# Optimization experiments

Measured on AMD Instinct MI355X. Metric: run time of the kernel, lower is better.

## Reference

```python
import jax, jax.numpy as jnp
import numpy as np

N_NODES = 50000
N_EDGES = 400000
N_TRAIN = 50000
IN_DIM = 128
HIDDEN = 512


def gcn_conv(x, W, b, src, dst, num_nodes):
    """PyG-style GCNConv: linear -> add self-loops -> sym-normalized scatter-add -> bias."""
    h = x @ W  # [N, out]
    loop = jnp.arange(num_nodes, dtype=src.dtype)
    src2 = jnp.concatenate([src, loop])  # self-loops appended
    dst2 = jnp.concatenate([dst, loop])
    ones = jnp.ones(src2.shape[0], dtype=h.dtype)
    deg = jax.ops.segment_sum(ones, dst2, num_segments=num_nodes)  # in-degree incl. self-loop
    dis = jnp.where(deg > 0, jax.lax.rsqrt(deg), 0.0)
    norm = dis[src2] * dis[dst2]  # [E+N]
    msgs = h[src2] * norm[:, None]  # [E+N, out] gather
    out = jax.ops.segment_sum(msgs, dst2, num_segments=num_nodes)  # scatter-add
    return out + b


def setup_inputs() -> dict:
    key = jax.random.key(0)
    ks = jax.random.split(key, 12)
    x = jax.random.normal(ks[0], (N_NODES, IN_DIM), dtype=jnp.float32)
    edge_index = jax.random.randint(ks[1], (2, N_EDGES), 0, N_NODES, dtype=jnp.int32)
    train_edge_id = jax.random.randint(ks[2], (N_TRAIN,), 0, N_EDGES, dtype=jnp.int32)
    def glorot(k, fi, fo):
        s = (6.0 / (fi + fo)) ** 0.5
        return jax.random.uniform(k, (fi, fo), jnp.float32, -s, s)
    return {
        "x": x,
        "edge_index": edge_index,
        "train_edge_id": train_edge_id,
        "W1": glorot(ks[3], IN_DIM, HIDDEN), "b1": jnp.zeros((HIDDEN,), jnp.float32),
        "W2": glorot(ks[4], HIDDEN, HIDDEN), "b2": jnp.zeros((HIDDEN,), jnp.float32),
        "W3": glorot(ks[5], HIDDEN, HIDDEN), "b3": jnp.zeros((HIDDEN,), jnp.float32),
        "fc2_W": glorot(ks[6], HIDDEN, 1), "fc2_b": jnp.zeros((1,), jnp.float32),
    }


def reference(x, edge_index, train_edge_id, W1, b1, W2, b2, W3, b3, fc2_W, fc2_b):
    src, dst = edge_index[0], edge_index[1]
    n = x.shape[0]
    h = jnp.tanh(gcn_conv(x, W1, b1, src, dst, n))
    h = jnp.tanh(gcn_conv(h, W2, b2, src, dst, n))
    h = jnp.tanh(gcn_conv(h, W3, b3, src, dst, n))
    # dropout is identity in eval mode
    node_id = edge_index[:, train_edge_id]  # [2, T]
    e = h[node_id[0]] * h[node_id[1]]  # [T, HIDDEN] edge gather + mul
    return e @ fc2_W + fc2_b  # [T, 1]
```

## Files before the change

### kernel.cpp

```cpp
#include <hip/hip_runtime.h>
#include <math.h>

#define N_NODES 50000
#define N_EDGES 400000
#define N_TRAIN 50000
#define IN_DIM  128
#define HIDDEN  512
#define M_PAD   50048
#define SCAN_B  196

typedef _Float16 f16;
typedef __attribute__((ext_vector_type(8))) _Float16 f16x8;
typedef __attribute__((ext_vector_type(4))) _Float16 f16x4;
typedef __attribute__((ext_vector_type(4))) float f32x4;


__global__ void count_dst_kernel(const int* __restrict__ dst, int* __restrict__ cnt) {
    int i = blockIdx.x * blockDim.x + threadIdx.x;
    if (i < N_EDGES) atomicAdd(&cnt[dst[i]], 1);
}

__global__ void dis_kernel(const int* __restrict__ cnt, float* __restrict__ dis) {
    int v = blockIdx.x * blockDim.x + threadIdx.x;
    if (v < N_NODES) dis[v] = rsqrtf(1.0f + (float)cnt[v]);
}

__global__ void scan1_kernel(const int* __restrict__ cnt, int* __restrict__ bsum) {
    __shared__ int red[256];
    int t = threadIdx.x, i = blockIdx.x * 256 + t;
    red[t] = (i < N_NODES) ? cnt[i] : 0;
    __syncthreads();
    for (int o = 128; o > 0; o >>= 1) {
        if (t < o) red[t] += red[t + o];
        __syncthreads();
    }
    if (t == 0) bsum[blockIdx.x] = red[0];
}

__global__ void scan2_kernel(const int* __restrict__ bsum, int* __restrict__ boff) {
    __shared__ int part[256];
    int t = threadIdx.x;
    int v = (t < SCAN_B) ? bsum[t] : 0;
    part[t] = v;
    __syncthreads();
    for (int o = 1; o < 256; o <<= 1) {
        int u = (t >= o) ? part[t - o] : 0;
        __syncthreads();
        part[t] += u;
        __syncthreads();
    }
    if (t < SCAN_B) boff[t] = part[t] - v;
}

__global__ void scan3_kernel(const int* __restrict__ cnt, const int* __restrict__ boff,
                             int* __restrict__ off) {
    __shared__ int part[256];
    int t = threadIdx.x, i = blockIdx.x * 256 + t;
    int v = (i < N_NODES) ? cnt[i] : 0;
    part[t] = v;
    __syncthreads();
    for (int o = 1; o < 256; o <<= 1) {
        int u = (t >= o) ? part[t - o] : 0;
        __syncthreads();
        part[t] += u;
        __syncthreads();
    }
    int excl = part[t] - v;
    int base = boff[blockIdx.x];
    if (i < N_NODES) off[i] = base + excl;
    if (i == N_NODES - 1) off[N_NODES] = base + excl + v;
}

__global__ void fill_csr_kernel(const int* __restrict__ src, const int* __restrict__ dst,
                                const int* __restrict__ off, int* __restrict__ cursor,
                                const float* __restrict__ dis,
                                int* __restrict__ csr_src, float* __restrict__ csr_w) {
    int i = blockIdx.x * blockDim.x + threadIdx.x;
    if (i < N_EDGES) {
        int d = dst[i], s = src[i];
        int p = atomicAdd(&cursor[d], 1);
        int idx = off[d] + p;
        csr_src[idx] = s;
        csr_w[idx] = dis[s];
    }
}

__global__ void convw_kernel(const float* __restrict__ W, f16* __restrict__ Bt, int K) {
    int idx = blockIdx.x * blockDim.x + threadIdx.x;
    if (idx >= K * HIDDEN) return;
    int k = idx / HIDDEN, n = idx % HIDDEN;
    Bt[(size_t)n * K + k] = (f16)W[(size_t)k * HIDDEN + n];
}

__global__ void agg1_kernel(const float* __restrict__ x, const float* __restrict__ dis,
                            const int* __restrict__ off, const int* __restrict__ csr_src,
                            const float* __restrict__ csr_w, f16* __restrict__ A) {
    const int TPN = 32;
    int node = blockIdx.x * 8 + threadIdx.x / TPN;
    if (node >= N_NODES) return;
    int t = threadIdx.x % TPN;
    float dv = dis[node];
    float w0 = dv * dv;
    float4 a = ((const float4*)(x + (size_t)node * IN_DIM))[t];
    float4 acc = make_float4(a.x * w0, a.y * w0, a.z * w0, a.w * w0);
    float4 acc1 = make_float4(0.f, 0.f, 0.f, 0.f);
    int s0 = off[node], s1 = off[node + 1];
    int k = s0;
    for (; k + 2 <= s1; k += 2) {
        int sa = csr_src[k], sb = csr_src[k + 1];
        float wa = csr_w[k] * dv, wb = csr_w[k + 1] * dv;
        float4 ba = ((const float4*)(x + (size_t)sa * IN_DIM))[t];
        float4 bb = ((const float4*)(x + (size_t)sb * IN_DIM))[t];
        acc.x = fmaf(wa, ba.x, acc.x);   acc.y = fmaf(wa, ba.y, acc.y);
        acc.z = fmaf(wa, ba.z, acc.z);   acc.w = fmaf(wa, ba.w, acc.w);
        acc1.x = fmaf(wb, bb.x, acc1.x); acc1.y = fmaf(wb, bb.y, acc1.y);
        acc1.z = fmaf(wb, bb.z, acc1.z); acc1.w = fmaf(wb, bb.w, acc1.w);
    }
    if (k < s1) {
        int sa = csr_src[k];
        float wa = csr_w[k] * dv;
        float4 ba = ((const float4*)(x + (size_t)sa * IN_DIM))[t];
        acc.x = fmaf(wa, ba.x, acc.x); acc.y = fmaf(wa, ba.y, acc.y);
        acc.z = fmaf(wa, ba.z, acc.z); acc.w = fmaf(wa, ba.w, acc.w);
    }
    f16x4 o;
    o.x = (f16)(acc.x + acc1.x); o.y = (f16)(acc.y + acc1.y);
    o.z = (f16)(acc.z + acc1.z); o.w = (f16)(acc.w + acc1.w);
    *(f16x4*)&A[(size_t)node * IN_DIM + t * 4] = o;
}

__global__ void agg_f16_kernel(const f16* __restrict__ h, const float* __restrict__ dis,
                               const int* __restrict__ off, const int* __restrict__ csr_src,
                               const float* __restrict__ csr_w, f16* __restrict__ A) {
    const int TPN = 64;
    int node = blockIdx.x * 4 + threadIdx.x / TPN;
    if (node >= N_NODES) return;
    int t = threadIdx.x % TPN;
    float dv = dis[node];
    float w0 = dv * dv;
    f16x8 a = *(const f16x8*)&h[(size_t)node * HIDDEN + t * 8];
    float acc0[8], acc1[8];
    #pragma unroll
    for (int j = 0; j < 8; j++) { acc0[j] = w0 * (float)a[j]; acc1[j] = 0.f; }
    int s0 = off[node], s1 = off[node + 1];
    int k = s0;
    for (; k + 8 <= s1; k += 8) {
        f16x8 b[8];
        float w[8];
        #pragma unroll
        for (int u = 0; u < 8; u++) {
            int su = csr_src[k + u];
            w[u] = csr_w[k + u] * dv;
            b[u] = *(const f16x8*)&h[(size_t)su * HIDDEN + t * 8];
        }
        #pragma unroll
        for (int j = 0; j < 8; j++) {
            acc0[j] = fmaf(w[0], (float)b[0][j], acc0[j]);
            acc1[j] = fmaf(w[1], (float)b[1][j], acc1[j]);
            acc0[j] = fmaf(w[2], (float)b[2][j], acc0[j]);
            acc1[j] = fmaf(w[3], (float)b[3][j], acc1[j]);
            acc0[j] = fmaf(w[4], (float)b[4][j], acc0[j]);
            acc1[j] = fmaf(w[5], (float)b[5][j], acc1[j]);
            acc0[j] = fmaf(w[6], (float)b[6][j], acc0[j]);
            acc1[j] = fmaf(w[7], (float)b[7][j], acc1[j]);
        }
    }
    if (k + 4 <= s1) {
        f16x8 b[4];
        float w[4];
        #pragma unroll
        for (int u = 0; u < 4; u++) {
            int su = csr_src[k + u];
            w[u] = csr_w[k + u] * dv;
            b[u] = *(const f16x8*)&h[(size_t)su * HIDDEN + t * 8];
        }
        #pragma unroll
        for (int j = 0; j < 8; j++) {
            acc0[j] = fmaf(w[0], (float)b[0][j], acc0[j]);
            acc1[j] = fmaf(w[1], (float)b[1][j], acc1[j]);
            acc0[j] = fmaf(w[2], (float)b[2][j], acc0[j]);
            acc1[j] = fmaf(w[3], (float)b[3][j], acc1[j]);
        }
        k += 4;
    }
    if (k + 2 <= s1) {
        int sa = csr_src[k], sb = csr_src[k + 1];
        float wa = csr_w[k] * dv, wb = csr_w[k + 1] * dv;
        f16x8 ba = *(const f16x8*)&h[(size_t)sa * HIDDEN + t * 8];
        f16x8 bb = *(const f16x8*)&h[(size_t)sb * HIDDEN + t * 8];
        #pragma unroll
        for (int j = 0; j < 8; j++) {
            acc0[j] = fmaf(wa, (float)ba[j], acc0[j]);
            acc1[j] = fmaf(wb, (float)bb[j], acc1[j]);
        }
        k += 2;
    }
    if (k < s1) {
        int sa = csr_src[k];
        float wa = csr_w[k] * dv;
        f16x8 ba = *(const f16x8*)&h[(size_t)sa * HIDDEN + t * 8];
        #pragma unroll
        for (int j = 0; j < 8; j++) acc0[j] = fmaf(wa, (float)ba[j], acc0[j]);
    }
    f16x8 o;
    #pragma unroll
    for (int j = 0; j < 8; j++) o[j] = (f16)(acc0[j] + acc1[j]);
    *(f16x8*)&A[(size_t)node * HIDDEN + t * 8] = o;
}

__global__ __launch_bounds__(256, 4) void gemm_mfma_kernel(
    const f16* __restrict__ A, const f16* __restrict__ Bt, const float* __restrict__ bias,
    f16* __restrict__ C, int M, int Kb) {
    __shared__ f16 smem[17408];
    f16* As = smem;
    f16* Bs = smem + 8192;
    int tid = threadIdx.x;
    int lane = tid & 63, wv = tid >> 6;
    int wr = wv >> 1, wc = wv & 1;

    int nwg = gridDim.x;
    int q = nwg >> 3, r = nwg & 7;
    int xcd = blockIdx.x & 7, pos = blockIdx.x >> 3;
    int wgid = (xcd < r ? xcd * (q + 1) : r * (q + 1) + (xcd - r) * q) + pos;
    int j0 = (wgid & 3) * 128;
    int i0 = (wgid >> 2) * 128;

    int l15 = lane & 15, l4 = lane >> 4;

    f32x4 acc[4][4];
    #pragma unroll
    for (int m = 0; m < 4; m++)
        #pragma unroll
        for (int n = 0; n < 4; n++)
            acc[m][n] = (f32x4){0.f, 0.f, 0.f, 0.f};

    const int nt = Kb / 64;
    for (int t = 0; t < nt; t++) {
        int k0 = t * 64;
        if (t) __syncthreads();
        #pragma unroll
        for (int i = 0; i < 4; i++) {
            int s = i * 256 + tid;
            int row = s >> 3, c8 = s & 7;
            int c8s = c8 ^ (row & 7);
            const f16* gp = A + (size_t)(i0 + row) * Kb + k0 + c8s * 8;
            f16* lp = &As[(i * 256 + wv * 64) * 8];
            __builtin_amdgcn_global_load_lds(
                (const __attribute__((address_space(1))) void*)gp,
                (__attribute__((address_space(3))) void*)lp, 16, 0, 0);
        }
        #pragma unroll
        for (int i = 0; i < 4; i++) {
            int s = i * 256 + tid;
            int row = s >> 3, c8 = s & 7;
            int c8s = c8 ^ (row & 7);
            const f16* gp = Bt + (size_t)(j0 + row) * Kb + k0 + c8s * 8;
            f16* lp = &Bs[(i * 256 + wv * 64) * 8];
            __builtin_amdgcn_global_load_lds(
                (const __attribute__((address_space(1))) void*)gp,
                (__attribute__((address_space(3))) void*)lp, 16, 0, 0);
        }
        __syncthreads();

        f16x8 af[4][2], bfr[4][2];
        #pragma unroll
        for (int m = 0; m < 4; m++) {
            int row = wr * 64 + m * 16 + l15;
            #pragma unroll
            for (int kk = 0; kk < 2; kk++) {
                int slot = (kk * 4 + l4) ^ (row & 7);
                af[m][kk] = *(const f16x8*)&As[row * 64 + slot * 8];
            }
        }
        #pragma unroll
        for (int n = 0; n < 4; n++) {
            int brow = wc * 64 + n * 16 + l15;
            #pragma unroll
            for (int kk = 0; kk < 2; kk++) {
                int slot = (kk * 4 + l4) ^ (brow & 7);
                bfr[n][kk] = *(const f16x8*)&Bs[brow * 64 + slot * 8];
            }
        }
        #pragma unroll
        for (int m = 0; m < 4; m++)
            #pragma unroll
            for (int n = 0; n < 4; n++)
                #pragma unroll
                for (int kk = 0; kk < 2; kk++)
                    acc[m][n] = __builtin_amdgcn_mfma_f32_16x16x32_f16(
                        af[m][kk], bfr[n][kk], acc[m][n], 0, 0, 0);
    }

    __syncthreads();
    #pragma unroll
    for (int m = 0; m < 4; m++) {
        #pragma unroll
        for (int n = 0; n < 4; n++) {
            int lcol = wc * 64 + n * 16 + l15;
            float bc = bias[j0 + lcol];
            #pragma unroll
            for (int rr = 0; rr < 4; rr++) {
                int lrow = wr * 64 + m * 16 + l4 * 4 + rr;
                smem[lrow * 136 + lcol] = (f16)tanhf(acc[m][n][rr] + bc);
            }
        }
    }
    __syncthreads();
    #pragma unroll
    for (int j = 0; j < 8; j++) {
        int qq = j * 256 + tid;
        int row = qq >> 4, c8 = qq & 15;
        int grow = i0 + row;
        if (grow < M)
            *(f16x8*)&C[(size_t)grow * HIDDEN + j0 + c8 * 8] =
                *(const f16x8*)&smem[row * 136 + c8 * 8];
    }
}

__global__ void edge_score_kernel(const f16* __restrict__ h,
                                  const int* __restrict__ src, const int* __restrict__ dst,
                                  const int* __restrict__ te, const float* __restrict__ wgt,
                                  const float* __restrict__ fc2b, float* __restrict__ out) {
    int wid = threadIdx.x / 64;
    int lane = threadIdx.x % 64;
    int e = blockIdx.x * 4 + wid;
    if (e >= N_TRAIN) return;
    int id = te[e];
    int a = src[id], b = dst[id];
    f16x8 ha = *(const f16x8*)&h[(size_t)a * HIDDEN + lane * 8];
    f16x8 hb = *(const f16x8*)&h[(size_t)b * HIDDEN + lane * 8];
    float4 w0 = *(const float4*)&wgt[lane * 8];
    float4 w1 = *(const float4*)&wgt[lane * 8 + 4];
    float acc = 0.f;
    acc += (float)ha[0] * (float)hb[0] * w0.x;
    acc += (float)ha[1] * (float)hb[1] * w0.y;
    acc += (float)ha[2] * (float)hb[2] * w0.z;
    acc += (float)ha[3] * (float)hb[3] * w0.w;
    acc += (float)ha[4] * (float)hb[4] * w1.x;
    acc += (float)ha[5] * (float)hb[5] * w1.y;
    acc += (float)ha[6] * (float)hb[6] * w1.z;
    acc += (float)ha[7] * (float)hb[7] * w1.w;
    #pragma unroll
    for (int o = 32; o > 0; o >>= 1) acc += __shfl_down(acc, o);
    if (lane == 0) out[e] = acc + fc2b[0];
}


extern "C" void kernel_launch(void* const* d_in, const int* in_sizes, int n_in,
                              void* d_out, int out_size, void* d_ws, size_t ws_size,
                              hipStream_t stream) {
    const float* x    = (const float*)d_in[0];
    const int*   eidx = (const int*)d_in[1];
    const int*   te   = (const int*)d_in[2];
    const float* W1   = (const float*)d_in[3];
    const float* b1   = (const float*)d_in[4];
    const float* W2   = (const float*)d_in[5];
    const float* b2   = (const float*)d_in[6];
    const float* W3   = (const float*)d_in[7];
    const float* b3   = (const float*)d_in[8];
    const float* fc2W = (const float*)d_in[9];
    const float* fc2b = (const float*)d_in[10];
    const int* srcp = eidx;
    const int* dstp = eidx + N_EDGES;

    char* ws = (char*)d_ws;
    size_t used = 0;
    auto alloc = [&](size_t bytes) {
        void* p = ws + used;
        used += (bytes + 255) / 256 * 256;
        return p;
    };
    int*   cnt     = (int*)alloc((size_t)N_NODES * 4);
    int*   off     = (int*)alloc((size_t)(N_NODES + 1) * 4);
    int*   cursor  = (int*)alloc((size_t)N_NODES * 4);
    int*   bsum    = (int*)alloc((size_t)SCAN_B * 4);
    int*   boff    = (int*)alloc((size_t)SCAN_B * 4);
    int*   csr_src = (int*)alloc((size_t)N_EDGES * 4);
    float* csr_w   = (float*)alloc((size_t)N_EDGES * 4);
    float* dis     = (float*)alloc((size_t)N_NODES * 4);
    f16* Bt1 = (f16*)alloc((size_t)HIDDEN * IN_DIM * 2);
    f16* Bt2 = (f16*)alloc((size_t)HIDDEN * HIDDEN * 2);
    f16* Bt3 = (f16*)alloc((size_t)HIDDEN * HIDDEN * 2);
    f16* GA  = (f16*)alloc((size_t)M_PAD * HIDDEN * 2);
    f16* F   = (f16*)alloc((size_t)M_PAD * HIDDEN * 2);

    if (used > ws_size) return;

    hipMemsetAsync(cnt, 0, (size_t)N_NODES * 4, stream);
    hipMemsetAsync(cursor, 0, (size_t)N_NODES * 4, stream);

    count_dst_kernel<<<(N_EDGES + 255) / 256, 256, 0, stream>>>(dstp, cnt);
    dis_kernel<<<(N_NODES + 255) / 256, 256, 0, stream>>>(cnt, dis);
    scan1_kernel<<<SCAN_B, 256, 0, stream>>>(cnt, bsum);
    scan2_kernel<<<1, 256, 0, stream>>>(bsum, boff);
    scan3_kernel<<<SCAN_B, 256, 0, stream>>>(cnt, boff, off);
    fill_csr_kernel<<<(N_EDGES + 255) / 256, 256, 0, stream>>>(srcp, dstp, off, cursor, dis,
                                                               csr_src, csr_w);

    convw_kernel<<<(IN_DIM * HIDDEN + 255) / 256, 256, 0, stream>>>(W1, Bt1, IN_DIM);
    convw_kernel<<<(HIDDEN * HIDDEN + 255) / 256, 256, 0, stream>>>(W2, Bt2, HIDDEN);
    convw_kernel<<<(HIDDEN * HIDDEN + 255) / 256, 256, 0, stream>>>(W3, Bt3, HIDDEN);

    int gemm_blocks = (HIDDEN / 128) * (M_PAD / 128);

    agg1_kernel<<<(N_NODES + 7) / 8, 256, 0, stream>>>(x, dis, off, csr_src, csr_w, GA);
    gemm_mfma_kernel<<<gemm_blocks, 256, 0, stream>>>(GA, Bt1, b1, F, N_NODES, IN_DIM);
    agg_f16_kernel<<<(N_NODES + 3) / 4, 256, 0, stream>>>(F, dis, off, csr_src, csr_w, GA);
    gemm_mfma_kernel<<<gemm_blocks, 256, 0, stream>>>(GA, Bt2, b2, F, N_NODES, HIDDEN);
    agg_f16_kernel<<<(N_NODES + 3) / 4, 256, 0, stream>>>(F, dis, off, csr_src, csr_w, GA);
    gemm_mfma_kernel<<<gemm_blocks, 256, 0, stream>>>(GA, Bt3, b3, F, N_NODES, HIDDEN);
    edge_score_kernel<<<(N_TRAIN + 3) / 4, 256, 0, stream>>>(F, srcp, dstp, te, fc2W, fc2b,
                                                             (float*)d_out);
}
```

Baseline: 357.8 us.

## Fuse preprocessing kernels, cast x to fp16, and use nontemporal stores

Merges the dis computation into the first scan pass and folds the block-offset scan into the final scan kernel. The three weight-conversion launches become one. x is cast to fp16 up front so the first aggregation reuses the templated fp16 gather kernel and moves half the bytes per neighbour. Stores from the aggregation and GEMM epilogue are made nontemporal. This cuts launch count and gather traffic, but adds an extra pass over x, and nontemporal stores may hurt when the next kernel reads the output soon after.

After: 359.3 us. Within noise of the previous version (+0.4%).

```diff
diff --git a/kernel.cpp b/kernel.cpp
--- a/kernel.cpp
+++ b/kernel.cpp
@@ -11,7 +11,6 @@
 
 typedef _Float16 f16;
 typedef __attribute__((ext_vector_type(8))) _Float16 f16x8;
-typedef __attribute__((ext_vector_type(4))) _Float16 f16x4;
 typedef __attribute__((ext_vector_type(4))) float f32x4;
 
 
@@ -20,15 +19,13 @@
     if (i < N_EDGES) atomicAdd(&cnt[dst[i]], 1);
 }
 
-__global__ void dis_kernel(const int* __restrict__ cnt, float* __restrict__ dis) {
-    int v = blockIdx.x * blockDim.x + threadIdx.x;
-    if (v < N_NODES) dis[v] = rsqrtf(1.0f + (float)cnt[v]);
-}
-
-__global__ void scan1_kernel(const int* __restrict__ cnt, int* __restrict__ bsum) {
+__global__ void scan1_dis_kernel(const int* __restrict__ cnt, int* __restrict__ bsum,
+                                 float* __restrict__ dis) {
     __shared__ int red[256];
     int t = threadIdx.x, i = blockIdx.x * 256 + t;
-    red[t] = (i < N_NODES) ? cnt[i] : 0;
+    int v = (i < N_NODES) ? cnt[i] : 0;
+    if (i < N_NODES) dis[i] = rsqrtf(1.0f + (float)v);
+    red[t] = v;
     __syncthreads();
     for (int o = 128; o > 0; o >>= 1) {
         if (t < o) red[t] += red[t + o];
@@ -37,10 +34,23 @@
     if (t == 0) bsum[blockIdx.x] = red[0];
 }
 
-__global__ void scan2_kernel(const int* __restrict__ bsum, int* __restrict__ boff) {
+__global__ void scan3_kernel(const int* __restrict__ cnt, const int* __restrict__ bsum,
+                             int* __restrict__ off) {
+    __shared__ int bpart[256];
     __shared__ int part[256];
     int t = threadIdx.x;
-    int v = (t < SCAN_B) ? bsum[t] : 0;
+    int bv = (t < SCAN_B) ? bsum[t] : 0;
+    bpart[t] = bv;
+    __syncthreads();
+    for (int o = 1; o < 256; o <<= 1) {
+        int u = (t >= o) ? bpart[t - o] : 0;
+        __syncthreads();
+        bpart[t] += u;
+        __syncthreads();
+    }
+    int base = (blockIdx.x > 0) ? bpart[blockIdx.x - 1] : 0;
+    int i = blockIdx.x * 256 + t;
+    int v = (i < N_NODES) ? cnt[i] : 0;
     part[t] = v;
     __syncthreads();
     for (int o = 1; o < 256; o <<= 1) {
@@ -49,24 +59,7 @@
         part[t] += u;
         __syncthreads();
     }
-    if (t < SCAN_B) boff[t] = part[t] - v;
-}
-
-__global__ void scan3_kernel(const int* __restrict__ cnt, const int* __restrict__ boff,
-                             int* __restrict__ off) {
-    __shared__ int part[256];
-    int t = threadIdx.x, i = blockIdx.x * 256 + t;
-    int v = (i < N_NODES) ? cnt[i] : 0;
-    part[t] = v;
-    __syncthreads();
-    for (int o = 1; o < 256; o <<= 1) {
-        int u = (t >= o) ? part[t - o] : 0;
-        __syncthreads();
-        part[t] += u;
-        __syncthreads();
-    }
     int excl = part[t] - v;
-    int base = boff[blockIdx.x];
     if (i < N_NODES) off[i] = base + excl;
     if (i == N_NODES - 1) off[N_NODES] = base + excl + v;
 }
@@ -85,60 +78,50 @@
     }
 }
 
-__global__ void convw_kernel(const float* __restrict__ W, f16* __restrict__ Bt, int K) {
+__global__ void convw_all_kernel(const float* __restrict__ W1, const float* __restrict__ W2,
+                                 const float* __restrict__ W3, f16* __restrict__ Bt1,
+                                 f16* __restrict__ Bt2, f16* __restrict__ Bt3) {
+    const int S1 = IN_DIM * HIDDEN;
+    const int S2 = S1 + HIDDEN * HIDDEN;
+    const int S3 = S2 + HIDDEN * HIDDEN;
     int idx = blockIdx.x * blockDim.x + threadIdx.x;
-    if (idx >= K * HIDDEN) return;
-    int k = idx / HIDDEN, n = idx % HIDDEN;
-    Bt[(size_t)n * K + k] = (f16)W[(size_t)k * HIDDEN + n];
-}
-
-__global__ void agg1_kernel(const float* __restrict__ x, const float* __restrict__ dis,
-                            const int* __restrict__ off, const int* __restrict__ csr_src,
-                            const float* __restrict__ csr_w, f16* __restrict__ A) {
-    const int TPN = 32;
-    int node = blockIdx.x * 8 + threadIdx.x / TPN;
+    if (idx >= S3) return;
+    if (idx < S1) {
+        int k = idx / HIDDEN, n = idx % HIDDEN;
+        Bt1[(size_t)n * IN_DIM + k] = (f16)W1[idx];
+    } else if (idx < S2) {
+        int j = idx - S1;
+        int k = j / HIDDEN, n = j % HIDDEN;
+        Bt2[(size_t)n * HIDDEN + k] = (f16)W2[j];
+    } else {
+        int j = idx - S2;
+        int k = j / HIDDEN, n = j % HIDDEN;
+        Bt3[(size_t)n * HIDDEN + k] = (f16)W3[j];
+    }
+}
+
+__global__ void xcast_kernel(const float* __restrict__ x, f16* __restrict__ XF) {
+    int i = blockIdx.x * blockDim.x + threadIdx.x;
+    if (i >= N_NODES * IN_DIM / 8) return;
+    const float4* p = (const float4*)x + (size_t)i * 2;
+    float4 a = p[0], b = p[1];
+    f16x8 o = {(f16)a.x, (f16)a.y, (f16)a.z, (f16)a.w,
+               (f16)b.x, (f16)b.y, (f16)b.z, (f16)b.w};
+    __builtin_nontemporal_store(o, (f16x8*)XF + i);
+}
+
+template <int D>
+__global__ void agg_kernel(const f16* __restrict__ h, const float* __restrict__ dis,
+                           const int* __restrict__ off, const int* __restrict__ csr_src,
+                           const float* __restrict__ csr_w, f16* __restrict__ A) {
+    const int TPN = D / 8;
+    const int NPB = 256 / TPN;
+    int node = blockIdx.x * NPB + threadIdx.x / TPN;
     if (node >= N_NODES) return;
     int t = threadIdx.x % TPN;
     float dv = dis[node];
     float w0 = dv * dv;
-    float4 a = ((const float4*)(x + (size_t)node * IN_DIM))[t];
-    float4 acc = make_float4(a.x * w0, a.y * w0, a.z * w0, a.w * w0);
-    float4 acc1 = make_float4(0.f, 0.f, 0.f, 0.f);
-    int s0 = off[node], s1 = off[node + 1];
-    int k = s0;
-    for (; k + 2 <= s1; k += 2) {
-        int sa = csr_src[k], sb = csr_src[k + 1];
-        float wa = csr_w[k] * dv, wb = csr_w[k + 1] * dv;
-        float4 ba = ((const float4*)(x + (size_t)sa * IN_DIM))[t];
-        float4 bb = ((const float4*)(x + (size_t)sb * IN_DIM))[t];
-        acc.x = fmaf(wa, ba.x, acc.x);   acc.y = fmaf(wa, ba.y, acc.y);
-        acc.z = fmaf(wa, ba.z, acc.z);   acc.w = fmaf(wa, ba.w, acc.w);
-        acc1.x = fmaf(wb, bb.x, acc1.x); acc1.y = fmaf(wb, bb.y, acc1.y);
-        acc1.z = fmaf(wb, bb.z, acc1.z); acc1.w = fmaf(wb, bb.w, acc1.w);
-    }
-    if (k < s1) {
-        int sa = csr_src[k];
-        float wa = csr_w[k] * dv;
-        float4 ba = ((const float4*)(x + (size_t)sa * IN_DIM))[t];
-        acc.x = fmaf(wa, ba.x, acc.x); acc.y = fmaf(wa, ba.y, acc.y);
-        acc.z = fmaf(wa, ba.z, acc.z); acc.w = fmaf(wa, ba.w, acc.w);
-    }
-    f16x4 o;
-    o.x = (f16)(acc.x + acc1.x); o.y = (f16)(acc.y + acc1.y);
-    o.z = (f16)(acc.z + acc1.z); o.w = (f16)(acc.w + acc1.w);
-    *(f16x4*)&A[(size_t)node * IN_DIM + t * 4] = o;
-}
-
-__global__ void agg_f16_kernel(const f16* __restrict__ h, const float* __restrict__ dis,
-                               const int* __restrict__ off, const int* __restrict__ csr_src,
-                               const float* __restrict__ csr_w, f16* __restrict__ A) {
-    const int TPN = 64;
-    int node = blockIdx.x * 4 + threadIdx.x / TPN;
-    if (node >= N_NODES) return;
-    int t = threadIdx.x % TPN;
-    float dv = dis[node];
-    float w0 = dv * dv;
-    f16x8 a = *(const f16x8*)&h[(size_t)node * HIDDEN + t * 8];
+    f16x8 a = *(const f16x8*)&h[(size_t)node * D + t * 8];
     float acc0[8], acc1[8];
     #pragma unroll
     for (int j = 0; j < 8; j++) { acc0[j] = w0 * (float)a[j]; acc1[j] = 0.f; }
@@ -151,7 +134,7 @@
         for (int u = 0; u < 8; u++) {
             int su = csr_src[k + u];
             w[u] = csr_w[k + u] * dv;
-            b[u] = *(const f16x8*)&h[(size_t)su * HIDDEN + t * 8];
+            b[u] = *(const f16x8*)&h[(size_t)su * D + t * 8];
         }
         #pragma unroll
         for (int j = 0; j < 8; j++) {
@@ -172,7 +155,7 @@
         for (int u = 0; u < 4; u++) {
             int su = csr_src[k + u];
             w[u] = csr_w[k + u] * dv;
-            b[u] = *(const f16x8*)&h[(size_t)su * HIDDEN + t * 8];
+            b[u] = *(const f16x8*)&h[(size_t)su * D + t * 8];
         }
         #pragma unroll
         for (int j = 0; j < 8; j++) {
@@ -186,8 +169,8 @@
     if (k + 2 <= s1) {
         int sa = csr_src[k], sb = csr_src[k + 1];
         float wa = csr_w[k] * dv, wb = csr_w[k + 1] * dv;
-        f16x8 ba = *(const f16x8*)&h[(size_t)sa * HIDDEN + t * 8];
-        f16x8 bb = *(const f16x8*)&h[(size_t)sb * HIDDEN + t * 8];
+        f16x8 ba = *(const f16x8*)&h[(size_t)sa * D + t * 8];
+        f16x8 bb = *(const f16x8*)&h[(size_t)sb * D + t * 8];
         #pragma unroll
         for (int j = 0; j < 8; j++) {
             acc0[j] = fmaf(wa, (float)ba[j], acc0[j]);
@@ -198,14 +181,14 @@
     if (k < s1) {
         int sa = csr_src[k];
         float wa = csr_w[k] * dv;
-        f16x8 ba = *(const f16x8*)&h[(size_t)sa * HIDDEN + t * 8];
+        f16x8 ba = *(const f16x8*)&h[(size_t)sa * D + t * 8];
         #pragma unroll
         for (int j = 0; j < 8; j++) acc0[j] = fmaf(wa, (float)ba[j], acc0[j]);
     }
     f16x8 o;
     #pragma unroll
     for (int j = 0; j < 8; j++) o[j] = (f16)(acc0[j] + acc1[j]);
-    *(f16x8*)&A[(size_t)node * HIDDEN + t * 8] = o;
+    __builtin_nontemporal_store(o, (f16x8*)&A[(size_t)node * D + t * 8]);
 }
 
 __global__ __launch_bounds__(256, 4) void gemm_mfma_kernel(
@@ -311,9 +294,10 @@
         int qq = j * 256 + tid;
         int row = qq >> 4, c8 = qq & 15;
         int grow = i0 + row;
-        if (grow < M)
-            *(f16x8*)&C[(size_t)grow * HIDDEN + j0 + c8 * 8] =
-                *(const f16x8*)&smem[row * 136 + c8 * 8];
+        if (grow < M) {
+            f16x8 v = *(const f16x8*)&smem[row * 136 + c8 * 8];
+            __builtin_nontemporal_store(v, (f16x8*)&C[(size_t)grow * HIDDEN + j0 + c8 * 8]);
+        }
     }
 }
 
@@ -374,13 +358,13 @@
     int*   off     = (int*)alloc((size_t)(N_NODES + 1) * 4);
     int*   cursor  = (int*)alloc((size_t)N_NODES * 4);
     int*   bsum    = (int*)alloc((size_t)SCAN_B * 4);
-    int*   boff    = (int*)alloc((size_t)SCAN_B * 4);
     int*   csr_src = (int*)alloc((size_t)N_EDGES * 4);
     float* csr_w   = (float*)alloc((size_t)N_EDGES * 4);
     float* dis     = (float*)alloc((size_t)N_NODES * 4);
     f16* Bt1 = (f16*)alloc((size_t)HIDDEN * IN_DIM * 2);
     f16* Bt2 = (f16*)alloc((size_t)HIDDEN * HIDDEN * 2);
     f16* Bt3 = (f16*)alloc((size_t)HIDDEN * HIDDEN * 2);
+    f16* XF  = (f16*)alloc((size_t)N_NODES * IN_DIM * 2);
     f16* GA  = (f16*)alloc((size_t)M_PAD * HIDDEN * 2);
     f16* F   = (f16*)alloc((size_t)M_PAD * HIDDEN * 2);
 
@@ -390,24 +374,23 @@
     hipMemsetAsync(cursor, 0, (size_t)N_NODES * 4, stream);
 
     count_dst_kernel<<<(N_EDGES + 255) / 256, 256, 0, stream>>>(dstp, cnt);
-    dis_kernel<<<(N_NODES + 255) / 256, 256, 0, stream>>>(cnt, dis);
-    scan1_kernel<<<SCAN_B, 256, 0, stream>>>(cnt, bsum);
-    scan2_kernel<<<1, 256, 0, stream>>>(bsum, boff);
-    scan3_kernel<<<SCAN_B, 256, 0, stream>>>(cnt, boff, off);
+    scan1_dis_kernel<<<SCAN_B, 256, 0, stream>>>(cnt, bsum, dis);
+    scan3_kernel<<<SCAN_B, 256, 0, stream>>>(cnt, bsum, off);
     fill_csr_kernel<<<(N_EDGES + 255) / 256, 256, 0, stream>>>(srcp, dstp, off, cursor, dis,
                                                                csr_src, csr_w);
-
-    convw_kernel<<<(IN_DIM * HIDDEN + 255) / 256, 256, 0, stream>>>(W1, Bt1, IN_DIM);
-    convw_kernel<<<(HIDDEN * HIDDEN + 255) / 256, 256, 0, stream>>>(W2, Bt2, HIDDEN);
-    convw_kernel<<<(HIDDEN * HIDDEN + 255) / 256, 256, 0, stream>>>(W3, Bt3, HIDDEN);
+    convw_all_kernel<<<(589824 + 255) / 256, 256, 0, stream>>>(W1, W2, W3, Bt1, Bt2, Bt3);
+    xcast_kernel<<<(N_NODES * IN_DIM / 8 + 255) / 256, 256, 0, stream>>>(x, XF);
 
     int gemm_blocks = (HIDDEN / 128) * (M_PAD / 128);
 
-    agg1_kernel<<<(N_NODES + 7) / 8, 256, 0, stream>>>(x, dis, off, csr_src, csr_w, GA);
+    agg_kernel<IN_DIM><<<(N_NODES + 15) / 16, 256, 0, stream>>>(XF, dis, off, csr_src,
+                                                                csr_w, GA);
     gemm_mfma_kernel<<<gemm_blocks, 256, 0, stream>>>(GA, Bt1, b1, F, N_NODES, IN_DIM);
-    agg_f16_kernel<<<(N_NODES + 3) / 4, 256, 0, stream>>>(F, dis, off, csr_src, csr_w, GA);
+    agg_kernel<HIDDEN><<<(N_NODES + 3) / 4, 256, 0, stream>>>(F, dis, off, csr_src,
+                                                              csr_w, GA);
     gemm_mfma_kernel<<<gemm_blocks, 256, 0, stream>>>(GA, Bt2, b2, F, N_NODES, HIDDEN);
-    agg_f16_kernel<<<(N_NODES + 3) / 4, 256, 0, stream>>>(F, dis, off, csr_src, csr_w, GA);
+    agg_kernel<HIDDEN><<<(N_NODES + 3) / 4, 256, 0, stream>>>(F, dis, off, csr_src,
+                                                              csr_w, GA);
     gemm_mfma_kernel<<<gemm_blocks, 256, 0, stream>>>(GA, Bt3, b3, F, N_NODES, HIDDEN);
     edge_score_kernel<<<(N_TRAIN + 3) / 4, 256, 0, stream>>>(F, srcp, dstp, te, fc2W, fc2b,
                                                              (float*)d_out);
```
